# Kernel tuning notes

Measured on AMD Instinct MI355X. Metric: run time of the kernel, lower is better.

Reference implementation:

```python
import jax, jax.numpy as jnp
import numpy as np

N = 8192          # num_nodes (adj.shape[0])
NFEAT = 1433      # Cora features
NHID = 64
NCLASS = 7
P_VEC_SIZE = N * (N + 1) // 2  # lower triangle incl. diagonal


def setup_inputs() -> dict:
    key = jax.random.key(0)
    k1, k2, k3, k4 = jax.random.split(key, 4)
    x = jax.random.normal(k1, (N, NFEAT), dtype=jnp.float32)
    # sparse symmetric 0/1 adjacency, avg degree ~33
    u = jax.random.uniform(k2, (N, N), dtype=jnp.float32)
    a = (u < 0.002).astype(jnp.float32)
    sub_adj = jnp.clip(a + a.T, 0.0, 1.0)
    sub_adj = sub_adj * (1.0 - jnp.eye(N, dtype=jnp.float32))  # no self loops
    # P_vec initialized to ones (edge_additions=False branch), minus eps as in reset_parameters
    P_vec = jnp.ones((P_VEC_SIZE,), dtype=jnp.float32)
    W1 = jax.random.normal(k3, (NFEAT, NHID), dtype=jnp.float32) / np.sqrt(NFEAT)
    b1 = jnp.zeros((NHID,), dtype=jnp.float32)
    W2 = jax.random.normal(k4, (NHID, NCLASS), dtype=jnp.float32) / np.sqrt(NHID)
    b2 = jnp.zeros((NCLASS,), dtype=jnp.float32)
    return {"x": x, "sub_adj": sub_adj, "P_vec": P_vec,
            "W1": W1, "b1": b1, "W2": W2, "b2": b2}


def _symm_from_vec(p_vec, n):
    # create_symm_matrix_from_vec: scatter vec into lower triangle (incl diag),
    # then mirror strict lower triangle to upper.
    il, jl = jnp.tril_indices(n)
    m = jnp.zeros((n, n), dtype=p_vec.dtype).at[il, jl].set(p_vec)
    return jnp.tril(m) + jnp.tril(m, -1).T


def reference(x, sub_adj, P_vec, W1, b1, W2, b2):
    n = sub_adj.shape[0]
    P_hat_symm = _symm_from_vec(P_vec, n)
    # A_tilde = sigmoid(P) * sub_adj + I  (edge_additions=False)
    A_tilde = jax.nn.sigmoid(P_hat_symm) * sub_adj + jnp.eye(n, dtype=sub_adj.dtype)
    # degree matrix is detached in the original forward
    d = jax.lax.stop_gradient(jnp.sum(A_tilde, axis=1))
    d_inv_sqrt = jnp.where(d > 0, d ** -0.5, 0.0)  # inf -> 0 guard
    # D^-1/2 A D^-1/2 (diag matmuls expressed as broadcasts)
    norm_adj = d_inv_sqrt[:, None] * A_tilde * d_inv_sqrt[None, :]
    # 2-layer GCN (pygcn GraphConvolution: adj @ (x @ W) + b); eval mode => dropout is identity
    h1 = jax.nn.relu(norm_adj @ (x @ W1) + b1)
    h2 = norm_adj @ (h1 @ W2) + b2
    return jax.nn.log_softmax(h2, axis=1)
```

## Files before the change

kernel.cpp:

```cpp
#include <hip/hip_runtime.h>
#include <hip/hip_bf16.h>
#include <math.h>

#define NN 8192
#define NFEAT 1433
#define NHID 64
#define NCLASS 7
#define CAP 96

#define KSPLIT 8
#define KCHUNK 192
#define KPAD 1440
#define NB_GEMM 1024
#define NB_BUILD 2048

typedef float f32x4 __attribute__((ext_vector_type(4)));
typedef short bf16x8 __attribute__((ext_vector_type(8)));

__device__ __forceinline__ ushort f2bf(float f) {
    __hip_bfloat16 h = __float2bfloat16(f);
    return *reinterpret_cast<ushort*>(&h);
}

__global__ __launch_bounds__(256) void k_prep(const float* __restrict__ W1,
                                              ushort* __restrict__ W1bfT) {
    int idx = blockIdx.x * 256 + threadIdx.x;
    if (idx >= KPAD * 64) return;
    int k = idx >> 6, c = idx & 63;
    W1bfT[(size_t)c * KPAD + k] = (k < NFEAT) ? f2bf(W1[(size_t)k * 64 + c]) : (ushort)0;
}

__global__ __launch_bounds__(256, 8) void k_fused(const float* __restrict__ adj,
                                                  const float* __restrict__ P,
                                                  const float* __restrict__ x,
                                                  const ushort* __restrict__ W1bfT,
                                                  float* __restrict__ dinv,
                                                  int* __restrict__ cnt,
                                                  int* __restrict__ cols,
                                                  float* __restrict__ vals,
                                                  float* __restrict__ part) {
    __shared__ __align__(16) union SMem {
        struct { ushort xa[64][40]; ushort wt[64][40]; } g;
        int bcols[4][CAP];
    } sm;

    const int t = threadIdx.x;
    const int b = blockIdx.x;
    const int rmod = b % 3;
    const int g = b / 3;

    if (rmod == 0) {
        const int tile = g >> 3;
        const int ks   = g & 7;
        const int m0 = tile * 64;
        const int k_begin = ks * KCHUNK;
        const int k_end   = (k_begin + KCHUNK < NFEAT) ? k_begin + KCHUNK : NFEAT;
        const int l = t & 63;
        const int w = t >> 6;

        const int sr  = t >> 2;
        const int sc8 = (t & 3) * 8;
        const float* xrow = x + (size_t)(m0 + sr) * NFEAT;
        const int wc  = t & 63;
        const int wk8 = (t >> 6) * 8;
        const ushort* wsrc = W1bfT + (size_t)wc * KPAD;
        const int arow = w * 16 + (l & 15);
        const int kb   = (l >> 4) * 8;

        f32x4 acc[4];
        #pragma unroll
        for (int ct = 0; ct < 4; ++ct) acc[ct] = (f32x4){0.f, 0.f, 0.f, 0.f};

        for (int k0 = k_begin; k0 < k_end; k0 += 32) {
            uint4 xp;
            {
                ushort u[8];
                #pragma unroll
                for (int jj = 0; jj < 8; ++jj) {
                    int k = k0 + sc8 + jj;
                    float f = (k < k_end) ? xrow[k] : 0.f;
                    u[jj] = f2bf(f);
                }
                xp.x = (unsigned)u[0] | ((unsigned)u[1] << 16);
                xp.y = (unsigned)u[2] | ((unsigned)u[3] << 16);
                xp.z = (unsigned)u[4] | ((unsigned)u[5] << 16);
                xp.w = (unsigned)u[6] | ((unsigned)u[7] << 16);
            }
            *(uint4*)(&sm.g.xa[sr][sc8]) = xp;
            *(uint4*)(&sm.g.wt[wc][wk8]) = *(const uint4*)(wsrc + k0 + wk8);
            __syncthreads();

            bf16x8 af = *(const bf16x8*)(&sm.g.xa[arow][kb]);
            #pragma unroll
            for (int ct = 0; ct < 4; ++ct) {
                bf16x8 bfr = *(const bf16x8*)(&sm.g.wt[ct * 16 + (l & 15)][kb]);
                acc[ct] = __builtin_amdgcn_mfma_f32_16x16x32_bf16(af, bfr, acc[ct], 0, 0, 0);
            }
            __syncthreads();
        }
        float* pout = part + (size_t)ks * NN * NHID;
        const int orow = m0 + w * 16 + ((l >> 4) << 2);
        const int ocol = l & 15;
        #pragma unroll
        for (int ct = 0; ct < 4; ++ct)
            #pragma unroll
            for (int rix = 0; rix < 4; ++rix)
                pout[(size_t)(orow + rix) * 64 + ct * 16 + ocol] = acc[ct][rix];
    } else {
        const int wave = t >> 6;
        const int lane = t & 63;
        const int bid  = 2 * g + (rmod - 1);
        const int row  = bid * 4 + wave;

        const f32x4* arow4 = (const f32x4*)(adj + (size_t)row * NN);
        const long tb = (long)row * (row + 1) / 2;
        const unsigned long long lt = (1ull << lane) - 1ull;
        const size_t rowCAP = (size_t)row * CAP;

        int base = 0;

        f32x4 buf[4];
        #pragma unroll
        for (int i = 0; i < 4; ++i)
            buf[i] = __builtin_nontemporal_load(&arow4[i * 64 + lane]);

        for (int sb = 0; sb < 8; ++sb) {
            f32x4 cur[4];
            #pragma unroll
            for (int i = 0; i < 4; ++i) cur[i] = buf[i];
            if (sb < 7) {
                #pragma unroll
                for (int i = 0; i < 4; ++i)
                    buf[i] = __builtin_nontemporal_load(&arow4[((sb + 1) * 4 + i) * 64 + lane]);
            }
            #pragma unroll
            for (int i = 0; i < 4; ++i) {
                const int jb = ((sb * 4 + i) * 64 + lane) * 4;
                #pragma unroll
                for (int s = 0; s < 4; ++s) {
                    bool nz = (cur[i][s] != 0.f);
                    unsigned long long mask = __ballot(nz);
                    if (nz) {
                        int j = jb + s;
                        int pos = base + __popcll(mask & lt);
                        if (pos < CAP) {
                            cols[rowCAP + pos] = j;
                            sm.bcols[wave][pos] = j;
                        }
                    }
                    base += __popcll(mask);
                }
            }
        }
        __syncthreads();

        const int c = (base < CAP) ? base : CAP;
        float dsum = 0.f;
        for (int k = lane; k < c; k += 64) {
            int j = sm.bcols[wave][k];
            long pidx = (j <= row) ? (tb + j) : ((long)j * (j + 1) / 2 + row);
            float p = P[pidx];
            float v = 1.f / (1.f + __expf(-p));
            vals[rowCAP + k] = v;
            dsum += v;
        }
        #pragma unroll
        for (int s = 32; s; s >>= 1) dsum += __shfl_xor(dsum, s, 64);
        if (lane == 0) {
            cnt[row]  = c;
            dinv[row] = 1.f / sqrtf(1.f + dsum);
        }
    }
}

__global__ __launch_bounds__(256) void k_reduce(const float* __restrict__ part,
                                                float* __restrict__ XW1) {
    const size_t i4 = (size_t)blockIdx.x * 256 + threadIdx.x;
    const f32x4* p4 = (const f32x4*)part;
    f32x4 s = p4[i4];
    #pragma unroll
    for (int ks = 1; ks < KSPLIT; ++ks)
        s += p4[(size_t)ks * (NN * NHID / 4) + i4];
    ((f32x4*)XW1)[i4] = s;
}

__global__ __launch_bounds__(256) void k_spmm1(const float* __restrict__ XW1,
                                               const float* __restrict__ dinv,
                                               const int* __restrict__ cnt,
                                               const int* __restrict__ cols,
                                               const float* __restrict__ vals,
                                               const float* __restrict__ b1,
                                               const float* __restrict__ W2,
                                               float* __restrict__ HW2) {
    const int wave = threadIdx.x >> 6;
    const int lane = threadIdx.x & 63;
    const int row  = blockIdx.x * 4 + wave;
    if (row >= NN) return;

    const float di = dinv[row];
    float acc = di * XW1[(size_t)row * NHID + lane];
    const int c = cnt[row];
    const int*   cp = cols + (size_t)row * CAP;
    const float* vp = vals + (size_t)row * CAP;

    int j0 = 0, j1 = 0; float v0 = 0.f, v1 = 0.f, w0 = 0.f, w1 = 0.f, d0 = 0.f, d1 = 0.f;
    if (c > 0) { j0 = cp[0]; v0 = vp[0]; w0 = XW1[(size_t)j0 * NHID + lane]; d0 = dinv[j0]; }
    if (c > 1) { j1 = cp[1]; v1 = vp[1]; w1 = XW1[(size_t)j1 * NHID + lane]; d1 = dinv[j1]; }
    for (int k = 0; k < c; ++k) {
        acc += v0 * d0 * w0;
        j0 = j1; v0 = v1; w0 = w1; d0 = d1;
        if (k + 2 < c) {
            int jn = cp[k + 2];
            j1 = jn; v1 = vp[k + 2];
            w1 = XW1[(size_t)jn * NHID + lane];
            d1 = dinv[jn];
        }
    }
    float h1 = di * acc + b1[lane];
    h1 = fmaxf(h1, 0.f);

    float o[NCLASS];
    #pragma unroll
    for (int cc = 0; cc < NCLASS; ++cc) o[cc] = h1 * W2[lane * NCLASS + cc];
    #pragma unroll
    for (int cc = 0; cc < NCLASS; ++cc)
        for (int s = 32; s; s >>= 1) o[cc] += __shfl_xor(o[cc], s, 64);
    if (lane == 0) {
        #pragma unroll
        for (int cc = 0; cc < NCLASS; ++cc)
            HW2[(size_t)row * NCLASS + cc] = o[cc];
    }
}

__global__ __launch_bounds__(256) void k_spmm2(const float* __restrict__ HW2,
                                               const float* __restrict__ dinv,
                                               const int* __restrict__ cnt,
                                               const int* __restrict__ cols,
                                               const float* __restrict__ vals,
                                               const float* __restrict__ b2,
                                               float* __restrict__ out) {
    const int wave = threadIdx.x >> 6;
    const int lane = threadIdx.x & 63;
    const int row  = blockIdx.x * 4 + wave;
    if (row >= NN) return;

    const int c = cnt[row];
    const int*   cp = cols + (size_t)row * CAP;
    const float* vp = vals + (size_t)row * CAP;
    float acc[NCLASS] = {};
    for (int k = lane; k < c; k += 64) {
        int j   = cp[k];
        float wgt = vp[k] * dinv[j];
        #pragma unroll
        for (int cc = 0; cc < NCLASS; ++cc)
            acc[cc] += wgt * HW2[(size_t)j * NCLASS + cc];
    }
    #pragma unroll
    for (int cc = 0; cc < NCLASS; ++cc)
        for (int s = 32; s; s >>= 1) acc[cc] += __shfl_xor(acc[cc], s, 64);

    if (lane == 0) {
        const float di = dinv[row];
        float h[NCLASS], m = -1e30f;
        #pragma unroll
        for (int cc = 0; cc < NCLASS; ++cc) {
            h[cc] = di * (acc[cc] + di * HW2[(size_t)row * NCLASS + cc]) + b2[cc];
            m = fmaxf(m, h[cc]);
        }
        float s = 0.f;
        #pragma unroll
        for (int cc = 0; cc < NCLASS; ++cc) s += expf(h[cc] - m);
        float lse = m + logf(s);
        #pragma unroll
        for (int cc = 0; cc < NCLASS; ++cc)
            out[(size_t)row * NCLASS + cc] = h[cc] - lse;
    }
}

extern "C" void kernel_launch(void* const* d_in, const int* in_sizes, int n_in,
                              void* d_out, int out_size, void* d_ws, size_t ws_size,
                              hipStream_t stream) {
    const float* x   = (const float*)d_in[0];
    const float* adj = (const float*)d_in[1];
    const float* P   = (const float*)d_in[2];
    const float* W1  = (const float*)d_in[3];
    const float* b1  = (const float*)d_in[4];
    const float* W2  = (const float*)d_in[5];
    const float* b2  = (const float*)d_in[6];
    float* out = (float*)d_out;

    char* ws = (char*)d_ws;
    size_t off = 0;
    float* dinv = (float*)(ws + off);  off += (size_t)NN * 4;
    int*   cnt  = (int*)  (ws + off);  off += (size_t)NN * 4;
    int*   cols = (int*)  (ws + off);  off += (size_t)NN * CAP * 4;
    float* vals = (float*)(ws + off);  off += (size_t)NN * CAP * 4;
    float* XW1  = (float*)(ws + off);  off += (size_t)NN * NHID * 4;
    float* HW2  = (float*)(ws + off);  off += (size_t)NN * NCLASS * 4;
    float* part = (float*)(ws + off);  off += (size_t)KSPLIT * NN * NHID * 4;
    ushort* W1bfT = (ushort*)(ws + off); off += (size_t)64 * KPAD * 2;

    k_prep<<<dim3(KPAD * 64 / 256), dim3(256), 0, stream>>>(W1, W1bfT);
    k_fused<<<dim3(NB_GEMM + NB_BUILD), dim3(256), 0, stream>>>(adj, P, x, W1bfT,
                                                                dinv, cnt, cols, vals, part);
    k_reduce<<<dim3(NN * NHID / 4 / 256), dim3(256), 0, stream>>>(part, XW1);
    k_spmm1<<<dim3(NN / 4), dim3(256), 0, stream>>>(XW1, dinv, cnt, cols, vals, b1, W2, HW2);
    k_spmm2<<<dim3(NN / 4), dim3(256), 0, stream>>>(HW2, dinv, cnt, cols, vals, b2, out);
}
```

Before: 128.5 us.

## Split adjacency row scan across four waves and drop W1 prep kernel

Each adjacency row is now scanned by a full 256-thread block, with each wave covering a quarter of the row, instead of one wave per row. Per-wave nonzero lists are merged through shared memory, and the degree sums are combined across waves. The separate W1 transpose/bf16 prep kernel is removed; the GEMM blocks read W1 fp32 directly and convert it to bf16 on the fly. Nontemporal loads become regular loads. This aims for more memory-level parallelism and one fewer launch, at the cost of strided uncoalesced W1 reads in the GEMM and a per-quarter cap of 48 nonzeros.

After: 143.4 us. 1.12x slower.

```diff
diff --git a/kernel.cpp b/kernel.cpp
--- a/kernel.cpp
+++ b/kernel.cpp
@@ -7,12 +7,12 @@
 #define NHID 64
 #define NCLASS 7
 #define CAP 96
+#define QCAP 48
 
 #define KSPLIT 8
 #define KCHUNK 192
-#define KPAD 1440
 #define NB_GEMM 1024
-#define NB_BUILD 2048
+#define NB_BUILD 8192
 
 typedef float f32x4 __attribute__((ext_vector_type(4)));
 typedef short bf16x8 __attribute__((ext_vector_type(8)));
@@ -22,18 +22,10 @@
     return *reinterpret_cast<ushort*>(&h);
 }
 
-__global__ __launch_bounds__(256) void k_prep(const float* __restrict__ W1,
-                                              ushort* __restrict__ W1bfT) {
-    int idx = blockIdx.x * 256 + threadIdx.x;
-    if (idx >= KPAD * 64) return;
-    int k = idx >> 6, c = idx & 63;
-    W1bfT[(size_t)c * KPAD + k] = (k < NFEAT) ? f2bf(W1[(size_t)k * 64 + c]) : (ushort)0;
-}
-
 __global__ __launch_bounds__(256, 8) void k_fused(const float* __restrict__ adj,
                                                   const float* __restrict__ P,
                                                   const float* __restrict__ x,
-                                                  const ushort* __restrict__ W1bfT,
+                                                  const float* __restrict__ W1,
                                                   float* __restrict__ dinv,
                                                   int* __restrict__ cnt,
                                                   int* __restrict__ cols,
@@ -41,17 +33,17 @@
                                                   float* __restrict__ part) {
     __shared__ __align__(16) union SMem {
         struct { ushort xa[64][40]; ushort wt[64][40]; } g;
-        int bcols[4][CAP];
+        struct { int qbuf[4][QCAP]; int qcnt[4]; float dpart[4]; } bl;
     } sm;
 
-    const int t = threadIdx.x;
-    const int b = blockIdx.x;
-    const int rmod = b % 3;
-    const int g = b / 3;
-
-    if (rmod == 0) {
-        const int tile = g >> 3;
-        const int ks   = g & 7;
+    const int t  = threadIdx.x;
+    const int b  = blockIdx.x;
+    const int r9 = b % 9;
+    const int q9 = b / 9;
+
+    if (r9 == 0) {
+        const int tile = q9 >> 3;
+        const int ks   = q9 & 7;
         const int m0 = tile * 64;
         const int k_begin = ks * KCHUNK;
         const int k_end   = (k_begin + KCHUNK < NFEAT) ? k_begin + KCHUNK : NFEAT;
@@ -63,7 +55,6 @@
         const float* xrow = x + (size_t)(m0 + sr) * NFEAT;
         const int wc  = t & 63;
         const int wk8 = (t >> 6) * 8;
-        const ushort* wsrc = W1bfT + (size_t)wc * KPAD;
         const int arow = w * 16 + (l & 15);
         const int kb   = (l >> 4) * 8;
 
@@ -78,8 +69,7 @@
                 #pragma unroll
                 for (int jj = 0; jj < 8; ++jj) {
                     int k = k0 + sc8 + jj;
-                    float f = (k < k_end) ? xrow[k] : 0.f;
-                    u[jj] = f2bf(f);
+                    u[jj] = f2bf((k < k_end) ? xrow[k] : 0.f);
                 }
                 xp.x = (unsigned)u[0] | ((unsigned)u[1] << 16);
                 xp.y = (unsigned)u[2] | ((unsigned)u[3] << 16);
@@ -87,7 +77,20 @@
                 xp.w = (unsigned)u[6] | ((unsigned)u[7] << 16);
             }
             *(uint4*)(&sm.g.xa[sr][sc8]) = xp;
-            *(uint4*)(&sm.g.wt[wc][wk8]) = *(const uint4*)(wsrc + k0 + wk8);
+            uint4 wp;
+            {
+                ushort u[8];
+                #pragma unroll
+                for (int jj = 0; jj < 8; ++jj) {
+                    int k = k0 + wk8 + jj;
+                    u[jj] = f2bf((k < k_end) ? W1[(size_t)k * 64 + wc] : 0.f);
+                }
+                wp.x = (unsigned)u[0] | ((unsigned)u[1] << 16);
+                wp.y = (unsigned)u[2] | ((unsigned)u[3] << 16);
+                wp.z = (unsigned)u[4] | ((unsigned)u[5] << 16);
+                wp.w = (unsigned)u[6] | ((unsigned)u[7] << 16);
+            }
+            *(uint4*)(&sm.g.wt[wc][wk8]) = wp;
             __syncthreads();
 
             bf16x8 af = *(const bf16x8*)(&sm.g.xa[arow][kb]);
@@ -109,66 +112,80 @@
     } else {
         const int wave = t >> 6;
         const int lane = t & 63;
-        const int bid  = 2 * g + (rmod - 1);
-        const int row  = bid * 4 + wave;
+        const int row  = q9 * 8 + (r9 - 1);
 
         const f32x4* arow4 = (const f32x4*)(adj + (size_t)row * NN);
         const long tb = (long)row * (row + 1) / 2;
         const unsigned long long lt = (1ull << lane) - 1ull;
         const size_t rowCAP = (size_t)row * CAP;
+        const int qb = wave * 512;
 
         int base = 0;
 
         f32x4 buf[4];
         #pragma unroll
         for (int i = 0; i < 4; ++i)
-            buf[i] = __builtin_nontemporal_load(&arow4[i * 64 + lane]);
-
-        for (int sb = 0; sb < 8; ++sb) {
+            buf[i] = arow4[qb + i * 64 + lane];
+
+        #pragma unroll
+        for (int sb = 0; sb < 2; ++sb) {
             f32x4 cur[4];
             #pragma unroll
             for (int i = 0; i < 4; ++i) cur[i] = buf[i];
-            if (sb < 7) {
+            if (sb == 0) {
                 #pragma unroll
                 for (int i = 0; i < 4; ++i)
-                    buf[i] = __builtin_nontemporal_load(&arow4[((sb + 1) * 4 + i) * 64 + lane]);
+                    buf[i] = arow4[qb + (4 + i) * 64 + lane];
             }
             #pragma unroll
             for (int i = 0; i < 4; ++i) {
-                const int jb = ((sb * 4 + i) * 64 + lane) * 4;
+                const int jb = (qb + (sb * 4 + i) * 64 + lane) * 4;
                 #pragma unroll
                 for (int s = 0; s < 4; ++s) {
                     bool nz = (cur[i][s] != 0.f);
                     unsigned long long mask = __ballot(nz);
                     if (nz) {
-                        int j = jb + s;
                         int pos = base + __popcll(mask & lt);
-                        if (pos < CAP) {
-                            cols[rowCAP + pos] = j;
-                            sm.bcols[wave][pos] = j;
-                        }
+                        if (pos < QCAP) sm.bl.qbuf[wave][pos] = jb + s;
                     }
                     base += __popcll(mask);
                 }
             }
         }
+        if (lane == 0) sm.bl.qcnt[wave] = (base < QCAP) ? base : QCAP;
         __syncthreads();
 
-        const int c = (base < CAP) ? base : CAP;
+        int off = 0, ctot = 0;
+        #pragma unroll
+        for (int ww = 0; ww < 4; ++ww) {
+            int qc = sm.bl.qcnt[ww];
+            if (ww < wave) off += qc;
+            ctot += qc;
+        }
+        if (ctot > CAP) ctot = CAP;
+
+        const int myq = sm.bl.qcnt[wave];
         float dsum = 0.f;
-        for (int k = lane; k < c; k += 64) {
-            int j = sm.bcols[wave][k];
+        if (lane < myq) {
+            int j = sm.bl.qbuf[wave][lane];
             long pidx = (j <= row) ? (tb + j) : ((long)j * (j + 1) / 2 + row);
             float p = P[pidx];
             float v = 1.f / (1.f + __expf(-p));
-            vals[rowCAP + k] = v;
-            dsum += v;
+            int pos = off + lane;
+            if (pos < CAP) {
+                cols[rowCAP + pos] = j;
+                vals[rowCAP + pos] = v;
+            }
+            dsum = v;
         }
         #pragma unroll
         for (int s = 32; s; s >>= 1) dsum += __shfl_xor(dsum, s, 64);
-        if (lane == 0) {
-            cnt[row]  = c;
-            dinv[row] = 1.f / sqrtf(1.f + dsum);
+        if (lane == 0) sm.bl.dpart[wave] = dsum;
+        __syncthreads();
+        if (t == 0) {
+            float ds = sm.bl.dpart[0] + sm.bl.dpart[1] + sm.bl.dpart[2] + sm.bl.dpart[3];
+            cnt[row]  = ctot;
+            dinv[row] = 1.f / sqrtf(1.f + ds);
         }
     }
 }
@@ -298,10 +315,8 @@
     float* XW1  = (float*)(ws + off);  off += (size_t)NN * NHID * 4;
     float* HW2  = (float*)(ws + off);  off += (size_t)NN * NCLASS * 4;
     float* part = (float*)(ws + off);  off += (size_t)KSPLIT * NN * NHID * 4;
-    ushort* W1bfT = (ushort*)(ws + off); off += (size_t)64 * KPAD * 2;
-
-    k_prep<<<dim3(KPAD * 64 / 256), dim3(256), 0, stream>>>(W1, W1bfT);
-    k_fused<<<dim3(NB_GEMM + NB_BUILD), dim3(256), 0, stream>>>(adj, P, x, W1bfT,
+
+    k_fused<<<dim3(NB_GEMM + NB_BUILD), dim3(256), 0, stream>>>(adj, P, x, W1,
                                                                 dinv, cnt, cols, vals, part);
     k_reduce<<<dim3(NN * NHID / 4 / 256), dim3(256), 0, stream>>>(part, XW1);
     k_spmm1<<<dim3(NN / 4), dim3(256), 0, stream>>>(XW1, dinv, cnt, cols, vals, b1, W2, HW2);
```
